# Kernel tuning notes

Measured on AMD Instinct MI355X. Metric: run time of the kernel, lower is better.

## Reference

```python
import jax, jax.numpy as jnp
import numpy as np

B, E, S, H = 8, 1024, 2048, 16  # batch, embed_dim, seq_len, n_heads
D = E // H                       # per-head hidden dim


def setup_inputs() -> dict:
    key = jax.random.key(0)
    k1, k2 = jax.random.split(key)
    x = jax.random.normal(k1, (B, E, S), dtype=jnp.float32)
    weight = jax.random.normal(k2, (H, S), dtype=jnp.float32)  # nn.Parameter(torch.randn)
    bias = jnp.zeros((H, S), dtype=jnp.float32)                # nn.Parameter(torch.zeros)
    return {"x": x, "weight": weight, "bias": bias}


def _vector_to_matrix(v):
    # v: (H, S) -> M: (H, S, S), M[h, i, j] = v[h, j - i] if j >= i else 0
    h, m = v.shape
    i = jnp.arange(m)[:, None]
    j = jnp.arange(m)[None, :]
    off = j - i  # negative offsets wrap (same as torch fancy indexing) but are masked out
    return jnp.where(j >= i, v[:, off], jnp.zeros((), dtype=v.dtype))


def reference(x, weight, bias):
    b, e, s = x.shape
    h = weight.shape[0]
    d = e // h
    M = _vector_to_matrix(weight)  # (H, S, S)
    # Original: x.view(B,H,D,S).reshape(B*H,D,S) paired with W.repeat_interleave(B,0),
    # i.e. flat index k uses M[k // B]. Group the flat B*H axis into H contiguous
    # blocks of size B so each block shares one Toeplitz matrix (no (B*H,S,S) blowup).
    xg = x.reshape(b * h, d, s).reshape(h, b, d, s)  # block m = M[m]
    out = jnp.einsum('mbds,mst->mbdt', xg, M) + bias[:, None, None, :]
    return out.reshape(b, e, s)
```

## Files before the change

### kernel.cpp

```cpp
#include <hip/hip_runtime.h>
#include <hip/hip_bf16.h>

#define SEQ    2048
#define NHEAD  16
#define RPH    512
#define BK     64
#define NTH    256

#define WSTRIDE 2184
#define ABUF_E  2048
#define WCOP_E  (2 * ABUF_E)
#define TOT_E   (WCOP_E + 8 * WSTRIDE)

typedef float  f32x4  __attribute__((ext_vector_type(4)));
typedef __bf16 bf16x8 __attribute__((ext_vector_type(8)));

struct PF { float4 v0, v1; };

__device__ __forceinline__ unsigned f2bf(float f) {
    union { __hip_bfloat16 h; unsigned short u; } cv;
    cv.h = __float2bfloat16(f);
    return (unsigned)cv.u;
}

__device__ __forceinline__ uint4 pack8u(float4 a, float4 b) {
    union { bf16x8 v; uint4 u; } r;
    r.v[0] = (__bf16)a.x; r.v[1] = (__bf16)a.y;
    r.v[2] = (__bf16)a.z; r.v[3] = (__bf16)a.w;
    r.v[4] = (__bf16)b.x; r.v[5] = (__bf16)b.y;
    r.v[6] = (__bf16)b.z; r.v[7] = (__bf16)b.w;
    return r.u;
}

#define MFMA16(a, b, c) __builtin_amdgcn_mfma_f32_16x16x32_bf16((a), (b), (c), 0, 0, 0)

#define LOADPF(P, CH)                                                         \
  { const float* g_ = Xp + (size_t)(CH) * BK;                                 \
    P.v0 = *(const float4*)g_;                                                \
    P.v1 = *(const float4*)(g_ + 4); }

#define WRITEA(AB, P)  { *(uint4*)((AB) + wb0) = pack8u(P.v0, P.v1); }

#define KSTEPQ(ABC, KS, P)                                                    \
  { const int kb_ = (64 * (KS) + kq16) ^ swz;                                 \
    bf16x8 af0 = *(const bf16x8*)((ABC) + Arow0 + kb_);                       \
    bf16x8 af1 = *(const bf16x8*)((ABC) + Arow1 + kb_);                       \
    acc[0][0] = MFMA16(af0, bw[((P)+2*(KS)-0)&15], acc[0][0]);                \
    acc[1][0] = MFMA16(af1, bw[((P)+2*(KS)-0)&15], acc[1][0]);                \
    acc[0][1] = MFMA16(af0, bw[((P)+2*(KS)-1)&15], acc[0][1]);                \
    acc[1][1] = MFMA16(af1, bw[((P)+2*(KS)-1)&15], acc[1][1]);                \
    acc[0][2] = MFMA16(af0, bw[((P)+2*(KS)-2)&15], acc[0][2]);                \
    acc[1][2] = MFMA16(af1, bw[((P)+2*(KS)-2)&15], acc[1][2]);                \
    acc[0][3] = MFMA16(af0, bw[((P)+2*(KS)-3)&15], acc[0][3]);                \
    acc[1][3] = MFMA16(af1, bw[((P)+2*(KS)-3)&15], acc[1][3]);                \
    acc[0][4] = MFMA16(af0, bw[((P)+2*(KS)-4)&15], acc[0][4]);                \
    acc[1][4] = MFMA16(af1, bw[((P)+2*(KS)-4)&15], acc[1][4]);                \
    acc[0][5] = MFMA16(af0, bw[((P)+2*(KS)-5)&15], acc[0][5]);                \
    acc[1][5] = MFMA16(af1, bw[((P)+2*(KS)-5)&15], acc[1][5]);                \
    acc[0][6] = MFMA16(af0, bw[((P)+2*(KS)-6)&15], acc[0][6]);                \
    acc[1][6] = MFMA16(af1, bw[((P)+2*(KS)-6)&15], acc[1][6]);                \
    acc[0][7] = MFMA16(af0, bw[((P)+2*(KS)-7)&15], acc[0][7]);                \
    acc[1][7] = MFMA16(af1, bw[((P)+2*(KS)-7)&15], acc[1][7]); }

#define CHUNKBODY(CH, P, ABC, ABN)                                            \
  {                                                                           \
    WRITEA(ABN, pf);                         \
    if ((CH) + 2 < nch) LOADPF(pf, (CH) + 2);                                 \
    if ((CH) < nchw) {                                                        \
      __builtin_amdgcn_s_setprio(1);                                          \
      KSTEPQ(ABC, 0, P);                                                      \
      bw[((P)+1)&15] = *(const bf16x8*)(wcB + 64 * (CH) + 16);                \
      bw[((P)+2)&15] = *(const bf16x8*)(wcB + 64 * (CH) + 32);                \
      KSTEPQ(ABC, 1, P);                                                      \
      __builtin_amdgcn_s_setprio(0);                                          \
    }                                                                         \
    if ((CH) + 1 < nchw) {                                                    \
      bw[((P)+3)&15] = *(const bf16x8*)(wcB + 64 * (CH) + 48);                \
      bw[((P)+4)&15] = *(const bf16x8*)(wcB + 64 * (CH) + 64);                \
    }                                                                         \
    asm volatile("s_waitcnt lgkmcnt(0)\n\ts_barrier" ::: "memory");           \
  }

__global__ __launch_bounds__(NTH, 2) void mixer_kernel(
    const float* __restrict__ x, const float* __restrict__ wgt,
    const float* __restrict__ bias, float* __restrict__ out)
{
    __shared__ unsigned short smem[TOT_E] __attribute__((aligned(16)));
    char* ab0 = (char*)smem;
    char* ab1 = (char*)smem + ABUF_E * 2;
    unsigned short* wc = smem + WCOP_E;

    const int tid  = threadIdx.x;
    const int lane = tid & 63;
    const int tb   = tid >> 6;

    const int bid  = blockIdx.x;
    const int m    = (bid & 7) + 8 * ((bid >> 3) & 1);
    const int rt   = (bid >> 4) & 15;
    const int pc   = bid >> 8;
    const int qA   = pc ? 2 : 3;
    const int qB   = pc ? 1 : 0;

    const float* Xb = x   + (size_t)(m * RPH + rt * 32) * SEQ;
    float*       Ob = out + (size_t)(m * RPH + rt * 32) * SEQ;
    const float* wr = wgt  + m * SEQ;
    const float* br = bias + m * SEQ;

    const int srow = tid >> 3;
    const int wsw  = (srow & 7) << 4;
    const int wb0  = srow * 128 + (((tid & 7) * 16) ^ wsw);
    const float* Xp = Xb + (size_t)srow * SEQ + (tid & 7) * 8;

    PF pf;
    LOADPF(pf, 0);

    {
        const int t8 = tid * 8;
        const float* g = wr + (2040 - t8);
        float4 lo = *(const float4*)g;
        float4 hi = *(const float4*)(g + 4);
        uint4 v;
        v.x = f2bf(hi.w) | (f2bf(hi.z) << 16);
        v.y = f2bf(hi.y) | (f2bf(hi.x) << 16);
        v.z = f2bf(lo.w) | (f2bf(lo.z) << 16);
        v.w = f2bf(lo.y) | (f2bf(lo.x) << 16);
        *(uint4*)(smem + 8 + t8) = v;
        if (tid < 21) {
            uint4 z = {0u, 0u, 0u, 0u};
            unsigned short* dst = (tid == 0) ? smem
                                 : smem + 8 + 2048 + (tid - 1) * 8;
            *(uint4*)dst = z;
        }
    }
    __syncthreads();

    #pragma unroll
    for (int c = 0; c < 8; ++c) {
        for (int grp = tid; grp < WSTRIDE / 8; grp += NTH) {
            const int i = grp * 8;
            uint4 g0 = *(const uint4*)(smem + 8 + i - 8);
            uint4 g1 = *(const uint4*)(smem + 8 + i);
            unsigned d[9] = {g0.x, g0.y, g0.z, g0.w,
                             g1.x, g1.y, g1.z, g1.w, 0u};
            const int qd = (16 - 2 * c) >> 2;
            uint4 o;
            if (c & 1) {
                o.x = (d[qd]     >> 16) | (d[qd + 1] << 16);
                o.y = (d[qd + 1] >> 16) | (d[qd + 2] << 16);
                o.z = (d[qd + 2] >> 16) | (d[qd + 3] << 16);
                o.w = (d[qd + 3] >> 16) | (d[qd + 4] << 16);
            } else {
                o.x = d[qd];     o.y = d[qd + 1];
                o.z = d[qd + 2]; o.w = d[qd + 3];
            }
            *(uint4*)(wc + c * WSTRIDE + i) = o;
        }
    }
    __syncthreads();

    const int col_low = lane & 15;
    const int kq      = lane >> 4;
    const int kq16    = kq * 16;
    const int swz     = (col_low & 7) << 4;
    const int cpy     = (col_low + 1) & 7;
    const int BcBase  = cpy * WSTRIDE + cpy + 2047 - col_low + 8 * kq;
    const int Arow0   = col_low * 128;
    const int Arow1   = (col_low + 16) * 128;

    for (int h = 0; h < 2; ++h) {
        const int q    = h ? qB : qA;
        const int nch  = 8 * q + 8;
        const int nchw = 8 * q + 2 * tb + 2;
        const int t0w  = 512 * q + 128 * tb;
        const unsigned short* wcB = wc + (BcBase - t0w);

        if (h) LOADPF(pf, 0);

        bf16x8 bw[16];
        #pragma unroll
        for (int w = -7; w <= 0; ++w)
            bw[w & 15] = *(const bf16x8*)(wcB + 16 * w);

        WRITEA(ab0, pf);
        LOADPF(pf, 1);
        asm volatile("s_waitcnt lgkmcnt(0)\n\ts_barrier" ::: "memory");

        f32x4 acc[2][8] = {};
        for (int ch = 0; ch < nch; ch += 4) {
            CHUNKBODY(ch,      0, ab0, ab1);
            CHUNKBODY(ch + 1,  4, ab1, ab0);
            CHUNKBODY(ch + 2,  8, ab0, ab1);
            CHUNKBODY(ch + 3, 12, ab1, ab0);
        }

        #pragma unroll
        for (int c = 0; c < 8; ++c) {
            const int colg = t0w + 16 * c + col_low;
            const float bv = br[colg];
            #pragma unroll
            for (int a = 0; a < 2; ++a) {
                const int rowl = 16 * a + 4 * kq;
                #pragma unroll
                for (int rr = 0; rr < 4; ++rr)
                    Ob[(size_t)(rowl + rr) * SEQ + colg] = acc[a][c][rr] + bv;
            }
        }
    }
}

extern "C" void kernel_launch(void* const* d_in, const int* in_sizes, int n_in,
                              void* d_out, int out_size, void* d_ws, size_t ws_size,
                              hipStream_t stream) {
    const float* x  = (const float*)d_in[0];
    const float* w  = (const float*)d_in[1];
    const float* bs = (const float*)d_in[2];
    float* out = (float*)d_out;
    dim3 grid(512);
    dim3 block(NTH);
    hipLaunchKernelGGL(mixer_kernel, grid, block, 0, stream, x, w, bs, out);
}
```

Before: 44.00 us.

## Process two K-chunks per barrier with four LDS A-buffers and doubled prefetch

Restructures the main loop so each barrier-separated step computes two 64-wide K chunks instead of one. It uses four LDS staging buffers and two register prefetch sets, loading chunks four and five ahead. This halves the number of block-wide barriers and deepens the global-load pipeline. In exchange it raises LDS usage by 8 KB per block and adds register pressure, which may hurt occupancy at launch_bounds(256,2).

```diff
diff --git a/kernel.cpp b/kernel.cpp
--- a/kernel.cpp
+++ b/kernel.cpp
@@ -9,7 +9,7 @@
 
 #define WSTRIDE 2184
 #define ABUF_E  2048
-#define WCOP_E  (2 * ABUF_E)
+#define WCOP_E  (4 * ABUF_E)
 #define TOT_E   (WCOP_E + 8 * WSTRIDE)
 
 typedef float  f32x4  __attribute__((ext_vector_type(4)));
@@ -62,21 +62,33 @@
     acc[0][7] = MFMA16(af0, bw[((P)+2*(KS)-7)&15], acc[0][7]);                \
     acc[1][7] = MFMA16(af1, bw[((P)+2*(KS)-7)&15], acc[1][7]); }
 
-#define CHUNKBODY(CH, P, ABC, ABN)                                            \
+#define SUPER(CH, P, C0, C1, N0, N1)                                          \
   {                                                                           \
-    WRITEA(ABN, pf);                         \
-    if ((CH) + 2 < nch) LOADPF(pf, (CH) + 2);                                 \
+    WRITEA(N0, pfA);                                                          \
+    WRITEA(N1, pfB);                                                          \
+    if ((CH) + 4 < nch) LOADPF(pfA, (CH) + 4);                                \
+    if ((CH) + 5 < nch) LOADPF(pfB, (CH) + 5);                                \
     if ((CH) < nchw) {                                                        \
       __builtin_amdgcn_s_setprio(1);                                          \
-      KSTEPQ(ABC, 0, P);                                                      \
+      KSTEPQ(C0, 0, P);                                                       \
       bw[((P)+1)&15] = *(const bf16x8*)(wcB + 64 * (CH) + 16);                \
       bw[((P)+2)&15] = *(const bf16x8*)(wcB + 64 * (CH) + 32);                \
-      KSTEPQ(ABC, 1, P);                                                      \
+      KSTEPQ(C0, 1, P);                                                       \
       __builtin_amdgcn_s_setprio(0);                                          \
     }                                                                         \
     if ((CH) + 1 < nchw) {                                                    \
       bw[((P)+3)&15] = *(const bf16x8*)(wcB + 64 * (CH) + 48);                \
       bw[((P)+4)&15] = *(const bf16x8*)(wcB + 64 * (CH) + 64);                \
+      __builtin_amdgcn_s_setprio(1);                                          \
+      KSTEPQ(C1, 0, (P) + 4);                                                 \
+      bw[((P)+5)&15] = *(const bf16x8*)(wcB + 64 * (CH) + 80);                \
+      bw[((P)+6)&15] = *(const bf16x8*)(wcB + 64 * (CH) + 96);                \
+      KSTEPQ(C1, 1, (P) + 4);                                                 \
+      __builtin_amdgcn_s_setprio(0);                                          \
+    }                                                                         \
+    if ((CH) + 2 < nchw) {                                                    \
+      bw[((P)+7)&15] = *(const bf16x8*)(wcB + 64 * (CH) + 112);               \
+      bw[((P)+8)&15] = *(const bf16x8*)(wcB + 64 * (CH) + 128);               \
     }                                                                         \
     asm volatile("s_waitcnt lgkmcnt(0)\n\ts_barrier" ::: "memory");           \
   }
@@ -88,6 +100,8 @@
     __shared__ unsigned short smem[TOT_E] __attribute__((aligned(16)));
     char* ab0 = (char*)smem;
     char* ab1 = (char*)smem + ABUF_E * 2;
+    char* ab2 = (char*)smem + ABUF_E * 4;
+    char* ab3 = (char*)smem + ABUF_E * 6;
     unsigned short* wc = smem + WCOP_E;
 
     const int tid  = threadIdx.x;
@@ -111,8 +125,9 @@
     const int wb0  = srow * 128 + (((tid & 7) * 16) ^ wsw);
     const float* Xp = Xb + (size_t)srow * SEQ + (tid & 7) * 8;
 
-    PF pf;
-    LOADPF(pf, 0);
+    PF pfA, pfB;
+    LOADPF(pfA, 0);
+    LOADPF(pfB, 1);
 
     {
         const int t8 = tid * 8;
@@ -174,23 +189,23 @@
         const int t0w  = 512 * q + 128 * tb;
         const unsigned short* wcB = wc + (BcBase - t0w);
 
-        if (h) LOADPF(pf, 0);
+        if (h) { LOADPF(pfA, 0); LOADPF(pfB, 1); }
 
         bf16x8 bw[16];
         #pragma unroll
         for (int w = -7; w <= 0; ++w)
             bw[w & 15] = *(const bf16x8*)(wcB + 16 * w);
 
-        WRITEA(ab0, pf);
-        LOADPF(pf, 1);
+        WRITEA(ab0, pfA);
+        WRITEA(ab1, pfB);
+        LOADPF(pfA, 2);
+        LOADPF(pfB, 3);
         asm volatile("s_waitcnt lgkmcnt(0)\n\ts_barrier" ::: "memory");
 
         f32x4 acc[2][8] = {};
         for (int ch = 0; ch < nch; ch += 4) {
-            CHUNKBODY(ch,      0, ab0, ab1);
-            CHUNKBODY(ch + 1,  4, ab1, ab0);
-            CHUNKBODY(ch + 2,  8, ab0, ab1);
-            CHUNKBODY(ch + 3, 12, ab1, ab0);
+            SUPER(ch,     0, ab0, ab1, ab2, ab3);
+            SUPER(ch + 2, 8, ab2, ab3, ab0, ab1);
         }
 
         #pragma unroll
```

Result: no change. 44.44 us (+1.0%).
